# Kernel optimization log

Hardware: AMD Instinct MI355X
Metric: run time of the kernel (lower is better)

## Reference

```python
import jax, jax.numpy as jnp
import numpy as np

B, O, L, E = 8, 4, 1024, 1024
BETA = 512
NSEG = 12
OUT = 1


def setup_inputs() -> dict:
    key = jax.random.key(0)
    ks = jax.random.split(key, 8)
    hidden = jax.random.normal(ks[0], (B, O, L, E), jnp.float32)
    # strictly increasing boundaries in (1, L), shared across the O options (as in the torch code)
    raw = jnp.sort(jax.random.randint(ks[1], (B, NSEG), 2, L - NSEG), axis=-1)
    idx = raw + jnp.arange(NSEG, dtype=raw.dtype)
    s = 0.02
    Wp = jax.random.normal(ks[2], (E, 2 * BETA), jnp.float32) * s
    bp = jnp.zeros((2 * BETA,), jnp.float32)
    Wa0 = jax.random.normal(ks[3], (2 * BETA, BETA), jnp.float32) * s
    ba0 = jnp.zeros((BETA,), jnp.float32)
    Wa = jax.random.normal(ks[4], (BETA, BETA), jnp.float32) * s
    ba = jnp.zeros((BETA,), jnp.float32)
    Wl0 = jax.random.normal(ks[5], (8 * BETA, BETA), jnp.float32) * s
    bl0 = jnp.zeros((BETA,), jnp.float32)
    Wl = jax.random.normal(ks[6], (BETA, OUT), jnp.float32) * s
    bl = jnp.zeros((OUT,), jnp.float32)
    return dict(hidden=hidden, idx=idx, Wp=Wp, bp=bp, Wa0=Wa0, ba0=ba0,
                Wa=Wa, ba=ba, Wl0=Wl0, bl0=bl0, Wl=Wl, bl=bl)


def _seg_mean(P, starts, ends):
    # P: [B,O,L+1,E] exclusive prefix sums; starts/ends: [B,K] token offsets.
    s = jnp.take_along_axis(P, starts[:, None, :, None], axis=2)
    e = jnp.take_along_axis(P, ends[:, None, :, None], axis=2)
    cnt = (ends - starts).astype(P.dtype)[:, None, :, None]
    return (e - s) / cnt  # [B,O,K,E]


def _get_param(x, Wp, bp):
    e = 1.0 + jax.nn.relu(x @ Wp + bp)
    a, b = jnp.split(e, 2, axis=-1)
    return a, b


def _attn_pool(a, b, Wa0, ba0, Wa, ba):
    # attention-weighted reduction over axis -2 (the 'logic' operator)
    h = jax.nn.relu(jnp.concatenate([a, b], axis=-1) @ Wa0 + ba0)
    w = jax.nn.softmax(h @ Wa + ba, axis=-2)
    return (w * a).sum(axis=-2), (w * b).sum(axis=-2)


def reference(hidden, idx, Wp, bp, Wa0, ba0, Wa, ba, Wl0, bl0, Wl, bl):
    # ---- init_embed: ragged segment means via prefix sums (one pass, no host syncs)
    P = jnp.concatenate([jnp.zeros_like(hidden[:, :, :1]),
                         jnp.cumsum(hidden, axis=2)], axis=2)  # [B,O,L+1,E]
    ones = jnp.ones((idx.shape[0], 1), idx.dtype)
    starts_c = jnp.concatenate([ones, idx[:, :NSEG - 3]], axis=1)  # [B, NSEG-2]
    ends_c = idx[:, :NSEG - 2]
    ctx = _seg_mean(P, starts_c, ends_c)                                # [B,O,Nc,E]
    q = _seg_mean(P, idx[:, NSEG - 3:NSEG - 2], idx[:, NSEG - 2:NSEG - 1])[:, :, 0]
    o = _seg_mean(P, idx[:, NSEG - 2:NSEG - 1], idx[:, NSEG - 1:NSEG])[:, :, 0]
    allc = _seg_mean(P, ones, idx[:, NSEG - 3:NSEG - 2])[:, :, 0]       # [B,O,E]
    # ---- beta params for context segments
    a_c, b_c = _get_param(ctx, Wp, bp)                                  # [B,O,Nc,BETA]
    # intersection over segments
    ia, ib = _attn_pool(a_c, b_c, Wa0, ba0, Wa, ba)                     # [B,O,BETA]
    # renew: pair each segment with the intersection, pool over the pair axis
    pa = jnp.stack([a_c, jnp.broadcast_to(ia[:, :, None, :], a_c.shape)], axis=-2)
    pb = jnp.stack([b_c, jnp.broadcast_to(ib[:, :, None, :], b_c.shape)], axis=-2)
    na, nb = _attn_pool(pa, pb, Wa0, ba0, Wa, ba)                       # [B,O,Nc,BETA]
    # union: invert, attention-pool over segments, invert back
    ua, ub = _attn_pool(1.0 / na, 1.0 / nb, Wa0, ba0, Wa, ba)
    ua, ub = 1.0 / ua, 1.0 / ub                                         # [B,O,BETA]
    # ---- beta params for question / option / whole-context spans
    a_q, b_q = _get_param(q, Wp, bp)
    a_o, b_o = _get_param(o, Wp, bp)
    a_ac, b_ac = _get_param(allc, Wp, bp)
    # ---- classify head: concat 4 beta embeddings -> 8*BETA -> MLP -> logits
    cat = jnp.concatenate([ua, ub, a_ac, b_ac, a_o, b_o, a_q, b_q], axis=-1)
    h = jax.nn.relu(cat @ Wl0 + bl0)
    return h @ Wl + bl  # [B,O,OUT]
```

## Files before the change

### kernel.cpp

```cpp
#include <hip/hip_runtime.h>
#include <hip/hip_bf16.h>

#define B_    8
#define O_    4
#define L_    1024
#define E_    1024
#define BETA_ 512
#define NSEG_ 12
#define BO_   32
#define NCH_  16

enum : size_t {
  WS_SPART = 0,
  WS_X     = WS_SPART + (size_t)BO_ * NCH_ * 12 * E_,
  WS_P1P   = WS_X     + (size_t)BO_ * 13 * E_,
  WS_H1P   = WS_P1P   + (size_t)8  * BO_ * 13 * E_,
  WS_T1P   = WS_H1P   + (size_t)16 * BO_ * 10 * BETA_,
  WS_H2P   = WS_T1P   + (size_t)8  * BO_ * 10 * BETA_,
  WS_T2P   = WS_H2P   + (size_t)8  * BO_ * BETA_,
  WS_H3P   = WS_T2P   + (size_t)8  * BO_ * BETA_,
  WS_T3P   = WS_H3P   + (size_t)16 * BO_ * 10 * BETA_,
  WS_HFP   = WS_T3P   + (size_t)8  * BO_ * 10 * BETA_,
  WS_TE    = WS_HFP   + (size_t)32 * BO_ * BETA_,
  WS_T1B   = WS_TE    + (size_t)BO_ * 13 * E_,
  WS_IAB   = WS_T1B   + (size_t)BO_ * 10 * BETA_,
  WS_RN    = WS_IAB   + (size_t)BO_ * 2 * BETA_,
  WS_END   = WS_RN    + (size_t)BO_ * 10 * E_,
};

__device__ __forceinline__ float relu_(float v) { return v > 0.f ? v : 0.f; }

__global__ void k1_segsum(const float* __restrict__ hidden, const int* __restrict__ idx,
                          float* __restrict__ Spart) {
    const int chunk = blockIdx.x;
    const int bo = blockIdx.y;
    const int b = bo >> 2;
    int cuts[13];
    cuts[0] = 1;
#pragma unroll
    for (int i = 0; i < 12; ++i) cuts[i + 1] = idx[b * NSEG_ + i];
    const int e4 = threadIdx.x << 2;
    float* sp = Spart + ((size_t)(bo * NCH_ + chunk) * 12) * E_ + e4;
    const float4 z = make_float4(0.f, 0.f, 0.f, 0.f);
#pragma unroll
    for (int m = 0; m < 12; ++m) *reinterpret_cast<float4*>(sp + (size_t)m * E_) = z;
    const int l0 = chunk * 64;
    const int l1 = l0 + 64;
    int lo = l0 < 1 ? 1 : l0;
    const int hi = l1 < cuts[12] ? l1 : cuts[12];
    if (lo >= hi) return;
    const float* base = hidden + (size_t)bo * (L_ * E_) + e4;
    int j = 0;
    while (j < 11 && cuts[j + 1] <= lo) ++j;
    int l = lo;
    while (l < hi) {
        const int e2 = (j < 11 && cuts[j + 1] < hi) ? cuts[j + 1] : hi;
        float sx = 0.f, sy = 0.f, sz = 0.f, sw = 0.f;
        for (; l < e2; ++l) {
            const float4 v = *reinterpret_cast<const float4*>(base + (size_t)l * E_);
            sx += v.x; sy += v.y; sz += v.z; sw += v.w;
        }
        float4 s; s.x = sx; s.y = sy; s.z = sz; s.w = sw;
        *reinterpret_cast<float4*>(sp + (size_t)j * E_) = s;
        ++j;
    }
}

__global__ __launch_bounds__(256) void k2_means(
    const float* __restrict__ Spart, const int* __restrict__ idx,
    float* __restrict__ X) {
    const int bo = blockIdx.y;
    const int col = blockIdx.x * 256 + threadIdx.x;
    const int b = bo >> 2;
    int cuts[13];
    cuts[0] = 1;
#pragma unroll
    for (int i = 0; i < 12; ++i) cuts[i + 1] = idx[b * NSEG_ + i];
    const float* sp = Spart + (size_t)bo * NCH_ * 12 * E_ + col;
    float allc = 0.f;
#pragma unroll
    for (int m = 0; m < 12; ++m) {
        float s = 0.f;
#pragma unroll
        for (int ch = 0; ch < NCH_; ++ch) s += sp[((size_t)ch * 12 + m) * E_];
        X[((size_t)bo * 13 + m) * E_ + col] = s / (float)(cuts[m + 1] - cuts[m]);
        if (m < 10) allc += s;
    }
    X[((size_t)bo * 13 + 12) * E_ + col] = allc / (float)(cuts[10] - 1);
}

template<int M, int ML, int K, int N, int KC, int BOG, int XF, int NPART>
__global__ __launch_bounds__(256) void gemm_sk(
    const float* __restrict__ Xb, const float* __restrict__ xbias,
    const float* __restrict__ W, float* __restrict__ OUT,
    const float* __restrict__ A0, const float* __restrict__ A1,
    const float* __restrict__ A2, const float* __restrict__ A3,
    float* __restrict__ SIDE, float* __restrict__ SIDE2) {
    const int kidx = blockIdx.x;
    const int k0 = kidx * KC;
    const int bo0 = blockIdx.y * BOG;
    const int c = blockIdx.z * 256 + threadIdx.x;
    const int tid = threadIdx.x;
    __shared__ __align__(16) float xs[BOG * ML * KC];

    for (int i = tid; i < BOG * ML * KC; i += 256) {
        const int kk = i % KC;
        const int rm = i / KC;
        const int m = rm % ML;
        const int bb = rm / ML;
        const int bo = bo0 + bb;
        const int k = k0 + kk;
        float v;
        if constexpr (XF == 0) {
            v = Xb[((size_t)bo * ML + m) * K + k];
        } else if constexpr (XF == 1) {
            float s = xbias[k];
#pragma unroll
            for (int p = 0; p < NPART; ++p)
                s += Xb[(((size_t)p * BO_ + bo) * ML + m) * K + k];
            v = 1.f + relu_(s);
            SIDE[((size_t)bo * ML + m) * K + k] = v;
        } else if constexpr (XF == 2) {
            float s = xbias[k];
#pragma unroll
            for (int p = 0; p < NPART; ++p)
                s += Xb[(((size_t)p * BO_ + bo) * ML + m) * K + k];
            v = relu_(s);
        } else if constexpr (XF == 4) {
            const int col = k & 511, half = k >> 9;
            const float bac = A2[col];
            float t[10], mx = -1e30f;
#pragma unroll
            for (int j = 0; j < 10; ++j) {
                float s = bac;
#pragma unroll
                for (int p = 0; p < NPART; ++p)
                    s += A0[(((size_t)p * BO_ + bo) * 10 + j) * BETA_ + col];
                t[j] = s;
                mx = fmaxf(mx, s);
            }
            if (half == 0) {
#pragma unroll
                for (int j = 0; j < 10; ++j)
                    SIDE2[((size_t)bo * 10 + j) * BETA_ + col] = t[j];
            }
            float sw = 0.f, acc = 0.f;
#pragma unroll
            for (int j = 0; j < 10; ++j) {
                const float pj = expf(t[j] - mx);
                sw += pj;
                acc = fmaf(pj, A1[((size_t)bo * 13 + j) * E_ + half * BETA_ + col], acc);
            }
            v = acc / sw;
            SIDE[(size_t)bo * 1024 + k] = v;
        } else if constexpr (XF == 5) {
            const int col = k & 511, half = k >> 9;
            const float tj = A0[((size_t)bo * 10 + m) * BETA_ + col];
            float tI = A2[col];
#pragma unroll
            for (int p = 0; p < NPART; ++p)
                tI += A1[((size_t)p * BO_ + bo) * BETA_ + col];
            const float mx = fmaxf(tj, tI);
            const float e0 = expf(tj - mx);
            const float e1 = expf(tI - mx);
            const float ea = A3[((size_t)bo * 13 + m) * E_ + half * BETA_ + col];
            const float iv = SIDE2[(size_t)bo * 1024 + k];
            v = (e0 + e1) / (e0 * ea + e1 * iv);
            SIDE[((size_t)bo * 10 + m) * E_ + k] = v;
        } else {
            if (k < 1024) {
                const int col = k & 511, half = k >> 9;
                const float bac = A2[col];
                float t[10], mx = -1e30f;
#pragma unroll
                for (int j = 0; j < 10; ++j) {
                    float s = bac;
#pragma unroll
                    for (int p = 0; p < NPART; ++p)
                        s += A0[(((size_t)p * BO_ + bo) * 10 + j) * BETA_ + col];
                    t[j] = s;
                    mx = fmaxf(mx, s);
                }
                float sw = 0.f, acc = 0.f;
#pragma unroll
                for (int j = 0; j < 10; ++j) {
                    const float pj = expf(t[j] - mx);
                    sw += pj;
                    acc = fmaf(pj, A1[((size_t)bo * 10 + j) * E_ + k], acc);
                }
                v = sw / acc;
            } else {
                const int region = k >> 10;
                const int row = (region == 1) ? 12 : (region == 2) ? 11 : 10;
                v = A3[((size_t)bo * 13 + row) * E_ + (k & 1023)];
            }
        }
        xs[i] = v;
    }
    __syncthreads();

    float acc[BOG][M];
#pragma unroll
    for (int b = 0; b < BOG; ++b)
#pragma unroll
        for (int m = 0; m < M; ++m) acc[b][m] = 0.f;
    const float* __restrict__ wp = W + (size_t)k0 * N + c;
    for (int k4 = 0; k4 < KC / 4; ++k4) {
        const float w0 = wp[(size_t)(4 * k4 + 0) * N];
        const float w1 = wp[(size_t)(4 * k4 + 1) * N];
        const float w2 = wp[(size_t)(4 * k4 + 2) * N];
        const float w3 = wp[(size_t)(4 * k4 + 3) * N];
#pragma unroll
        for (int b = 0; b < BOG; ++b) {
#pragma unroll
            for (int m = 0; m < M; ++m) {
                const float4 xv = *reinterpret_cast<const float4*>(&xs[(b * ML + m) * KC + 4 * k4]);
                float a = acc[b][m];
                a = fmaf(xv.x, w0, a);
                a = fmaf(xv.y, w1, a);
                a = fmaf(xv.z, w2, a);
                a = fmaf(xv.w, w3, a);
                acc[b][m] = a;
            }
        }
    }
#pragma unroll
    for (int b = 0; b < BOG; ++b) {
        float* op = OUT + (((size_t)kidx * BO_ + bo0 + b) * M) * N + c;
#pragma unroll
        for (int m = 0; m < M; ++m) op[(size_t)m * N] = acc[b][m];
    }
}

__global__ void __launch_bounds__(512) k_final(
    const float* __restrict__ HFP, const float* __restrict__ bl0,
    const float* __restrict__ Wl, const float* __restrict__ bl,
    float* __restrict__ out) {
    const int bo = blockIdx.x;
    const int c = threadIdx.x;
    float s = bl0[c];
#pragma unroll
    for (int p = 0; p < 32; ++p) s += HFP[((size_t)p * BO_ + bo) * BETA_ + c];
    float partial = relu_(s) * Wl[c];
#pragma unroll
    for (int off = 32; off > 0; off >>= 1) partial += __shfl_down(partial, off, 64);
    __shared__ float red[8];
    if ((c & 63) == 0) red[c >> 6] = partial;
    __syncthreads();
    if (c == 0) out[bo] = red[0] + red[1] + red[2] + red[3] + red[4] + red[5] + red[6] + red[7] + bl[0];
}

extern "C" void kernel_launch(void* const* d_in, const int* in_sizes, int n_in,
                              void* d_out, int out_size, void* d_ws, size_t ws_size,
                              hipStream_t stream) {
    const float* hidden = (const float*)d_in[0];
    const int* idx = (const int*)d_in[1];
    const float* Wp  = (const float*)d_in[2];
    const float* bp  = (const float*)d_in[3];
    const float* Wa0 = (const float*)d_in[4];
    const float* ba0 = (const float*)d_in[5];
    const float* Wa  = (const float*)d_in[6];
    const float* ba  = (const float*)d_in[7];
    const float* Wl0 = (const float*)d_in[8];
    const float* bl0 = (const float*)d_in[9];
    const float* Wl  = (const float*)d_in[10];
    const float* bl  = (const float*)d_in[11];
    float* ws = (float*)d_ws;
    float* SPART = ws + WS_SPART;
    float* X     = ws + WS_X;
    float* P1P   = ws + WS_P1P;
    float* H1P   = ws + WS_H1P;
    float* T1P   = ws + WS_T1P;
    float* H2P   = ws + WS_H2P;
    float* T2P   = ws + WS_T2P;
    float* H3P   = ws + WS_H3P;
    float* T3P   = ws + WS_T3P;
    float* HFP   = ws + WS_HFP;
    float* TE    = ws + WS_TE;
    float* T1B   = ws + WS_T1B;
    float* IAB   = ws + WS_IAB;
    float* RN    = ws + WS_RN;
    const float* NUL = nullptr;

    k1_segsum<<<dim3(NCH_, BO_), 256, 0, stream>>>(hidden, idx, SPART);
    k2_means<<<dim3(4, BO_), 256, 0, stream>>>(SPART, idx, X);
    gemm_sk<13, 13, 1024, 1024, 128, 2, 0, 1>
        <<<dim3(8, 16, 4), 256, 0, stream>>>(X, NUL, Wp, P1P, NUL, NUL, NUL, NUL, nullptr, nullptr);
    gemm_sk<10, 13, 1024, 512, 64, 2, 1, 8>
        <<<dim3(16, 16, 2), 256, 0, stream>>>(P1P, bp, Wa0, H1P, NUL, NUL, NUL, NUL, TE, nullptr);
    gemm_sk<10, 10, 512, 512, 64, 2, 2, 16>
        <<<dim3(8, 16, 2), 256, 0, stream>>>(H1P, ba0, Wa, T1P, NUL, NUL, NUL, NUL, nullptr, nullptr);
    gemm_sk<1, 1, 1024, 512, 128, 8, 4, 8>
        <<<dim3(8, 4, 2), 256, 0, stream>>>(NUL, NUL, Wa0, H2P, T1P, TE, ba, NUL, IAB, T1B);
    gemm_sk<1, 1, 512, 512, 64, 8, 2, 8>
        <<<dim3(8, 4, 2), 256, 0, stream>>>(H2P, ba0, Wa, T2P, NUL, NUL, NUL, NUL, nullptr, nullptr);
    gemm_sk<10, 10, 1024, 512, 64, 2, 5, 8>
        <<<dim3(16, 16, 2), 256, 0, stream>>>(NUL, NUL, Wa0, H3P, T1B, T2P, ba, TE, RN, IAB);
    gemm_sk<10, 10, 512, 512, 64, 2, 2, 16>
        <<<dim3(8, 16, 2), 256, 0, stream>>>(H3P, ba0, Wa, T3P, NUL, NUL, NUL, NUL, nullptr, nullptr);
    gemm_sk<1, 1, 4096, 512, 128, 8, 6, 8>
        <<<dim3(32, 4, 2), 256, 0, stream>>>(NUL, NUL, Wl0, HFP, T3P, RN, ba, TE, nullptr, nullptr);
    k_final<<<BO_, 512, 0, stream>>>(HFP, bl0, Wl, bl, (float*)d_out);
}
```

Measured before the change: 164.9 us.

## Finer segment-sum chunks and full-N per-block GEMM tiles with more split-K

The segment-sum kernel now uses 64 chunks of 16 rows instead of 16 chunks of 64, dropping the zero-fill of partial buffers and using two independent accumulators per segment. The means kernel sums only the chunks that overlap each segment, so unwritten partials are never read. The GEMMs now have each block cover all N columns, with NC columns per thread and blockIdx.z removed, so the shared-memory X tile is loaded once rather than per column group. They use smaller K chunks and more split-K partitions to keep block counts up. The aim is more parallelism in the bandwidth-bound hidden-state reduction and less redundant X staging, at the cost of more partial-sum traffic and higher register pressure.

After: 550.4 us. 3.34x slower.

```diff
diff --git a/kernel.cpp b/kernel.cpp
--- a/kernel.cpp
+++ b/kernel.cpp
@@ -8,24 +8,24 @@
 #define BETA_ 512
 #define NSEG_ 12
 #define BO_   32
-#define NCH_  16
+#define NCH_  64
 
 enum : size_t {
   WS_SPART = 0,
   WS_X     = WS_SPART + (size_t)BO_ * NCH_ * 12 * E_,
   WS_P1P   = WS_X     + (size_t)BO_ * 13 * E_,
-  WS_H1P   = WS_P1P   + (size_t)8  * BO_ * 13 * E_,
+  WS_TE    = WS_P1P   + (size_t)16 * BO_ * 13 * E_,
+  WS_H1P   = WS_TE    + (size_t)BO_ * 13 * E_,
   WS_T1P   = WS_H1P   + (size_t)16 * BO_ * 10 * BETA_,
-  WS_H2P   = WS_T1P   + (size_t)8  * BO_ * 10 * BETA_,
-  WS_T2P   = WS_H2P   + (size_t)8  * BO_ * BETA_,
-  WS_H3P   = WS_T2P   + (size_t)8  * BO_ * BETA_,
+  WS_T1B   = WS_T1P   + (size_t)16 * BO_ * 10 * BETA_,
+  WS_IAB   = WS_T1B   + (size_t)BO_ * 10 * BETA_,
+  WS_H2P   = WS_IAB   + (size_t)BO_ * 2 * BETA_,
+  WS_T2P   = WS_H2P   + (size_t)16 * BO_ * BETA_,
+  WS_RN    = WS_T2P   + (size_t)16 * BO_ * BETA_,
+  WS_H3P   = WS_RN    + (size_t)BO_ * 10 * E_,
   WS_T3P   = WS_H3P   + (size_t)16 * BO_ * 10 * BETA_,
-  WS_HFP   = WS_T3P   + (size_t)8  * BO_ * 10 * BETA_,
-  WS_TE    = WS_HFP   + (size_t)32 * BO_ * BETA_,
-  WS_T1B   = WS_TE    + (size_t)BO_ * 13 * E_,
-  WS_IAB   = WS_T1B   + (size_t)BO_ * 10 * BETA_,
-  WS_RN    = WS_IAB   + (size_t)BO_ * 2 * BETA_,
-  WS_END   = WS_RN    + (size_t)BO_ * 10 * E_,
+  WS_HFP   = WS_T3P   + (size_t)16 * BO_ * 10 * BETA_,
+  WS_END   = WS_HFP   + (size_t)32 * BO_ * BETA_,
 };
 
 __device__ __forceinline__ float relu_(float v) { return v > 0.f ? v : 0.f; }
@@ -39,28 +39,33 @@
     cuts[0] = 1;
 #pragma unroll
     for (int i = 0; i < 12; ++i) cuts[i + 1] = idx[b * NSEG_ + i];
-    const int e4 = threadIdx.x << 2;
-    float* sp = Spart + ((size_t)(bo * NCH_ + chunk) * 12) * E_ + e4;
-    const float4 z = make_float4(0.f, 0.f, 0.f, 0.f);
-#pragma unroll
-    for (int m = 0; m < 12; ++m) *reinterpret_cast<float4*>(sp + (size_t)m * E_) = z;
-    const int l0 = chunk * 64;
-    const int l1 = l0 + 64;
+    const int l0 = chunk * 16;
+    const int l1 = l0 + 16;
     int lo = l0 < 1 ? 1 : l0;
     const int hi = l1 < cuts[12] ? l1 : cuts[12];
     if (lo >= hi) return;
+    const int e4 = threadIdx.x << 2;
     const float* base = hidden + (size_t)bo * (L_ * E_) + e4;
+    float* sp = Spart + (size_t)(bo * NCH_ + chunk) * 12 * E_ + e4;
     int j = 0;
     while (j < 11 && cuts[j + 1] <= lo) ++j;
     int l = lo;
     while (l < hi) {
         const int e2 = (j < 11 && cuts[j + 1] < hi) ? cuts[j + 1] : hi;
         float sx = 0.f, sy = 0.f, sz = 0.f, sw = 0.f;
-        for (; l < e2; ++l) {
+        float tx = 0.f, ty = 0.f, tz = 0.f, tw = 0.f;
+        for (; l + 1 < e2; l += 2) {
+            const float4 v0 = *reinterpret_cast<const float4*>(base + (size_t)l * E_);
+            const float4 v1 = *reinterpret_cast<const float4*>(base + (size_t)(l + 1) * E_);
+            sx += v0.x; sy += v0.y; sz += v0.z; sw += v0.w;
+            tx += v1.x; ty += v1.y; tz += v1.z; tw += v1.w;
+        }
+        if (l < e2) {
             const float4 v = *reinterpret_cast<const float4*>(base + (size_t)l * E_);
             sx += v.x; sy += v.y; sz += v.z; sw += v.w;
+            ++l;
         }
-        float4 s; s.x = sx; s.y = sy; s.z = sz; s.w = sw;
+        float4 s; s.x = sx + tx; s.y = sy + ty; s.z = sz + tz; s.w = sw + tw;
         *reinterpret_cast<float4*>(sp + (size_t)j * E_) = s;
         ++j;
     }
@@ -80,30 +85,31 @@
     float allc = 0.f;
 #pragma unroll
     for (int m = 0; m < 12; ++m) {
+        const int c0 = cuts[m] >> 4;
+        const int c1 = (cuts[m + 1] - 1) >> 4;
         float s = 0.f;
-#pragma unroll
-        for (int ch = 0; ch < NCH_; ++ch) s += sp[((size_t)ch * 12 + m) * E_];
+        for (int ch = c0; ch <= c1; ++ch) s += sp[((size_t)ch * 12 + m) * E_];
         X[((size_t)bo * 13 + m) * E_ + col] = s / (float)(cuts[m + 1] - cuts[m]);
         if (m < 10) allc += s;
     }
     X[((size_t)bo * 13 + 12) * E_ + col] = allc / (float)(cuts[10] - 1);
 }
 
-template<int M, int ML, int K, int N, int KC, int BOG, int XF, int NPART>
-__global__ __launch_bounds__(256) void gemm_sk(
+template<int M, int ML, int K, int N, int KC, int BOG, int NT, int XF, int NPART>
+__global__ __launch_bounds__(NT) void gemm_nc(
     const float* __restrict__ Xb, const float* __restrict__ xbias,
-    const float* __restrict__ W, float* __restrict__ OUT,
+    const float* __restrict__ W, float* __restrict__ OUTP,
     const float* __restrict__ A0, const float* __restrict__ A1,
     const float* __restrict__ A2, const float* __restrict__ A3,
     float* __restrict__ SIDE, float* __restrict__ SIDE2) {
+    constexpr int NC = N / NT;
     const int kidx = blockIdx.x;
     const int k0 = kidx * KC;
     const int bo0 = blockIdx.y * BOG;
-    const int c = blockIdx.z * 256 + threadIdx.x;
     const int tid = threadIdx.x;
     __shared__ __align__(16) float xs[BOG * ML * KC];
 
-    for (int i = tid; i < BOG * ML * KC; i += 256) {
+    for (int i = tid; i < BOG * ML * KC; i += NT) {
         const int kk = i % KC;
         const int rm = i / KC;
         const int m = rm % ML;
@@ -169,7 +175,7 @@
             SIDE[((size_t)bo * 10 + m) * E_ + k] = v;
         } else {
             if (k < 1024) {
-                const int col = k & 511, half = k >> 9;
+                const int col = k & 511;
                 const float bac = A2[col];
                 float t[10], mx = -1e30f;
 #pragma unroll
@@ -199,36 +205,45 @@
     }
     __syncthreads();
 
-    float acc[BOG][M];
+    float acc[BOG][M][NC];
 #pragma unroll
     for (int b = 0; b < BOG; ++b)
 #pragma unroll
-        for (int m = 0; m < M; ++m) acc[b][m] = 0.f;
-    const float* __restrict__ wp = W + (size_t)k0 * N + c;
+        for (int m = 0; m < M; ++m)
+#pragma unroll
+            for (int q = 0; q < NC; ++q) acc[b][m][q] = 0.f;
+    const float* __restrict__ wp = W + (size_t)k0 * N + tid;
     for (int k4 = 0; k4 < KC / 4; ++k4) {
-        const float w0 = wp[(size_t)(4 * k4 + 0) * N];
-        const float w1 = wp[(size_t)(4 * k4 + 1) * N];
-        const float w2 = wp[(size_t)(4 * k4 + 2) * N];
-        const float w3 = wp[(size_t)(4 * k4 + 3) * N];
+        float w[4][NC];
+#pragma unroll
+        for (int kk = 0; kk < 4; ++kk)
+#pragma unroll
+            for (int q = 0; q < NC; ++q)
+                w[kk][q] = wp[(size_t)(4 * k4 + kk) * N + q * NT];
 #pragma unroll
         for (int b = 0; b < BOG; ++b) {
 #pragma unroll
             for (int m = 0; m < M; ++m) {
                 const float4 xv = *reinterpret_cast<const float4*>(&xs[(b * ML + m) * KC + 4 * k4]);
-                float a = acc[b][m];
-                a = fmaf(xv.x, w0, a);
-                a = fmaf(xv.y, w1, a);
-                a = fmaf(xv.z, w2, a);
-                a = fmaf(xv.w, w3, a);
-                acc[b][m] = a;
+#pragma unroll
+                for (int q = 0; q < NC; ++q) {
+                    float a = acc[b][m][q];
+                    a = fmaf(xv.x, w[0][q], a);
+                    a = fmaf(xv.y, w[1][q], a);
+                    a = fmaf(xv.z, w[2][q], a);
+                    a = fmaf(xv.w, w[3][q], a);
+                    acc[b][m][q] = a;
+                }
             }
         }
     }
 #pragma unroll
     for (int b = 0; b < BOG; ++b) {
-        float* op = OUT + (((size_t)kidx * BO_ + bo0 + b) * M) * N + c;
-#pragma unroll
-        for (int m = 0; m < M; ++m) op[(size_t)m * N] = acc[b][m];
+        float* op = OUTP + (((size_t)kidx * BO_ + bo0 + b) * M) * N + tid;
+#pragma unroll
+        for (int m = 0; m < M; ++m)
+#pragma unroll
+            for (int q = 0; q < NC; ++q) op[(size_t)m * N + q * NT] = acc[b][m][q];
     }
 }
 
@@ -269,36 +284,36 @@
     float* SPART = ws + WS_SPART;
     float* X     = ws + WS_X;
     float* P1P   = ws + WS_P1P;
+    float* TE    = ws + WS_TE;
     float* H1P   = ws + WS_H1P;
     float* T1P   = ws + WS_T1P;
+    float* T1B   = ws + WS_T1B;
+    float* IAB   = ws + WS_IAB;
     float* H2P   = ws + WS_H2P;
     float* T2P   = ws + WS_T2P;
+    float* RN    = ws + WS_RN;
     float* H3P   = ws + WS_H3P;
     float* T3P   = ws + WS_T3P;
     float* HFP   = ws + WS_HFP;
-    float* TE    = ws + WS_TE;
-    float* T1B   = ws + WS_T1B;
-    float* IAB   = ws + WS_IAB;
-    float* RN    = ws + WS_RN;
     const float* NUL = nullptr;
 
     k1_segsum<<<dim3(NCH_, BO_), 256, 0, stream>>>(hidden, idx, SPART);
     k2_means<<<dim3(4, BO_), 256, 0, stream>>>(SPART, idx, X);
-    gemm_sk<13, 13, 1024, 1024, 128, 2, 0, 1>
-        <<<dim3(8, 16, 4), 256, 0, stream>>>(X, NUL, Wp, P1P, NUL, NUL, NUL, NUL, nullptr, nullptr);
-    gemm_sk<10, 13, 1024, 512, 64, 2, 1, 8>
-        <<<dim3(16, 16, 2), 256, 0, stream>>>(P1P, bp, Wa0, H1P, NUL, NUL, NUL, NUL, TE, nullptr);
-    gemm_sk<10, 10, 512, 512, 64, 2, 2, 16>
-        <<<dim3(8, 16, 2), 256, 0, stream>>>(H1P, ba0, Wa, T1P, NUL, NUL, NUL, NUL, nullptr, nullptr);
-    gemm_sk<1, 1, 1024, 512, 128, 8, 4, 8>
-        <<<dim3(8, 4, 2), 256, 0, stream>>>(NUL, NUL, Wa0, H2P, T1P, TE, ba, NUL, IAB, T1B);
-    gemm_sk<1, 1, 512, 512, 64, 8, 2, 8>
-        <<<dim3(8, 4, 2), 256, 0, stream>>>(H2P, ba0, Wa, T2P, NUL, NUL, NUL, NUL, nullptr, nullptr);
-    gemm_sk<10, 10, 1024, 512, 64, 2, 5, 8>
-        <<<dim3(16, 16, 2), 256, 0, stream>>>(NUL, NUL, Wa0, H3P, T1B, T2P, ba, TE, RN, IAB);
-    gemm_sk<10, 10, 512, 512, 64, 2, 2, 16>
-        <<<dim3(8, 16, 2), 256, 0, stream>>>(H3P, ba0, Wa, T3P, NUL, NUL, NUL, NUL, nullptr, nullptr);
-    gemm_sk<1, 1, 4096, 512, 128, 8, 6, 8>
-        <<<dim3(32, 4, 2), 256, 0, stream>>>(NUL, NUL, Wl0, HFP, T3P, RN, ba, TE, nullptr, nullptr);
+    gemm_nc<13, 13, 1024, 1024, 64, 2, 256, 0, 1>
+        <<<dim3(16, 16), 256, 0, stream>>>(X, NUL, Wp, P1P, NUL, NUL, NUL, NUL, nullptr, nullptr);
+    gemm_nc<10, 13, 1024, 512, 64, 2, 128, 1, 16>
+        <<<dim3(16, 16), 128, 0, stream>>>(P1P, bp, Wa0, H1P, NUL, NUL, NUL, NUL, TE, nullptr);
+    gemm_nc<10, 10, 512, 512, 32, 2, 128, 2, 16>
+        <<<dim3(16, 16), 128, 0, stream>>>(H1P, ba0, Wa, T1P, NUL, NUL, NUL, NUL, nullptr, nullptr);
+    gemm_nc<1, 1, 1024, 512, 64, 8, 128, 4, 16>
+        <<<dim3(16, 4), 128, 0, stream>>>(NUL, NUL, Wa0, H2P, T1P, TE, ba, NUL, IAB, T1B);
+    gemm_nc<1, 1, 512, 512, 32, 8, 128, 2, 16>
+        <<<dim3(16, 4), 128, 0, stream>>>(H2P, ba0, Wa, T2P, NUL, NUL, NUL, NUL, nullptr, nullptr);
+    gemm_nc<10, 10, 1024, 512, 64, 2, 128, 5, 16>
+        <<<dim3(16, 16), 128, 0, stream>>>(NUL, NUL, Wa0, H3P, T1B, T2P, ba, TE, RN, IAB);
+    gemm_nc<10, 10, 512, 512, 32, 2, 128, 2, 16>
+        <<<dim3(16, 16), 128, 0, stream>>>(H3P, ba0, Wa, T3P, NUL, NUL, NUL, NUL, nullptr, nullptr);
+    gemm_nc<1, 1, 4096, 512, 128, 8, 128, 6, 16>
+        <<<dim3(32, 4), 128, 0, stream>>>(NUL, NUL, Wl0, HFP, T3P, RN, ba, TE, nullptr, nullptr);
     k_final<<<BO_, 512, 0, stream>>>(HFP, bl0, Wl, bl, (float*)d_out);
 }
```

## Split softmax-pool prologues out of GEMM staging into separate small kernels

Applied to the files above, without the earlier changes.

The attention softmax pooling that was recomputed inside the X-staging prologue of two split-K GEMMs (every column tile redid the 10-way softmax for its k chunk) moves into dedicated kernels, t_iab and t_cat. These write their pooled vectors to workspace once, and the GEMMs then load plain X. This removes redundant exp/reduction work repeated across N-tiles, at the cost of two extra launches and a round trip through global memory. The first projection GEMM also changes its BO grouping from 2 to 4 and halves its grid.

New measurement: 178.8 us. 8.4% more time.

```diff
diff --git a/kernel.cpp b/kernel.cpp
--- a/kernel.cpp
+++ b/kernel.cpp
@@ -25,7 +25,8 @@
   WS_T1B   = WS_TE    + (size_t)BO_ * 13 * E_,
   WS_IAB   = WS_T1B   + (size_t)BO_ * 10 * BETA_,
   WS_RN    = WS_IAB   + (size_t)BO_ * 2 * BETA_,
-  WS_END   = WS_RN    + (size_t)BO_ * 10 * E_,
+  WS_CAT   = WS_RN    + (size_t)BO_ * 10 * E_,
+  WS_END   = WS_CAT   + (size_t)BO_ * 8 * BETA_,
 };
 
 __device__ __forceinline__ float relu_(float v) { return v > 0.f ? v : 0.f; }
@@ -126,34 +127,7 @@
             for (int p = 0; p < NPART; ++p)
                 s += Xb[(((size_t)p * BO_ + bo) * ML + m) * K + k];
             v = relu_(s);
-        } else if constexpr (XF == 4) {
-            const int col = k & 511, half = k >> 9;
-            const float bac = A2[col];
-            float t[10], mx = -1e30f;
-#pragma unroll
-            for (int j = 0; j < 10; ++j) {
-                float s = bac;
-#pragma unroll
-                for (int p = 0; p < NPART; ++p)
-                    s += A0[(((size_t)p * BO_ + bo) * 10 + j) * BETA_ + col];
-                t[j] = s;
-                mx = fmaxf(mx, s);
-            }
-            if (half == 0) {
-#pragma unroll
-                for (int j = 0; j < 10; ++j)
-                    SIDE2[((size_t)bo * 10 + j) * BETA_ + col] = t[j];
-            }
-            float sw = 0.f, acc = 0.f;
-#pragma unroll
-            for (int j = 0; j < 10; ++j) {
-                const float pj = expf(t[j] - mx);
-                sw += pj;
-                acc = fmaf(pj, A1[((size_t)bo * 13 + j) * E_ + half * BETA_ + col], acc);
-            }
-            v = acc / sw;
-            SIDE[(size_t)bo * 1024 + k] = v;
-        } else if constexpr (XF == 5) {
+        } else {
             const int col = k & 511, half = k >> 9;
             const float tj = A0[((size_t)bo * 10 + m) * BETA_ + col];
             float tI = A2[col];
@@ -167,33 +141,6 @@
             const float iv = SIDE2[(size_t)bo * 1024 + k];
             v = (e0 + e1) / (e0 * ea + e1 * iv);
             SIDE[((size_t)bo * 10 + m) * E_ + k] = v;
-        } else {
-            if (k < 1024) {
-                const int col = k & 511, half = k >> 9;
-                const float bac = A2[col];
-                float t[10], mx = -1e30f;
-#pragma unroll
-                for (int j = 0; j < 10; ++j) {
-                    float s = bac;
-#pragma unroll
-                    for (int p = 0; p < NPART; ++p)
-                        s += A0[(((size_t)p * BO_ + bo) * 10 + j) * BETA_ + col];
-                    t[j] = s;
-                    mx = fmaxf(mx, s);
-                }
-                float sw = 0.f, acc = 0.f;
-#pragma unroll
-                for (int j = 0; j < 10; ++j) {
-                    const float pj = expf(t[j] - mx);
-                    sw += pj;
-                    acc = fmaf(pj, A1[((size_t)bo * 10 + j) * E_ + k], acc);
-                }
-                v = sw / acc;
-            } else {
-                const int region = k >> 10;
-                const int row = (region == 1) ? 12 : (region == 2) ? 11 : 10;
-                v = A3[((size_t)bo * 13 + row) * E_ + (k & 1023)];
-            }
         }
         xs[i] = v;
     }
@@ -230,6 +177,73 @@
 #pragma unroll
         for (int m = 0; m < M; ++m) op[(size_t)m * N] = acc[b][m];
     }
+}
+
+__global__ void __launch_bounds__(512) t_iab(
+    const float* __restrict__ T1P, const float* __restrict__ ba,
+    const float* __restrict__ TE, float* __restrict__ T1B,
+    float* __restrict__ IAB) {
+    const int bo = blockIdx.x;
+    const int c = threadIdx.x;
+    const float bac = ba[c];
+    float t[10], mx = -1e30f;
+#pragma unroll
+    for (int j = 0; j < 10; ++j) {
+        float s = bac;
+#pragma unroll
+        for (int p = 0; p < 8; ++p)
+            s += T1P[(((size_t)p * BO_ + bo) * 10 + j) * BETA_ + c];
+        t[j] = s;
+        T1B[((size_t)bo * 10 + j) * BETA_ + c] = s;
+        mx = fmaxf(mx, s);
+    }
+    float p[10], sw = 0.f;
+#pragma unroll
+    for (int j = 0; j < 10; ++j) { p[j] = expf(t[j] - mx); sw += p[j]; }
+    float ia = 0.f, ib = 0.f;
+#pragma unroll
+    for (int j = 0; j < 10; ++j) {
+        ia = fmaf(p[j], TE[((size_t)bo * 13 + j) * E_ + c], ia);
+        ib = fmaf(p[j], TE[((size_t)bo * 13 + j) * E_ + BETA_ + c], ib);
+    }
+    IAB[(size_t)bo * 1024 + c] = ia / sw;
+    IAB[(size_t)bo * 1024 + BETA_ + c] = ib / sw;
+}
+
+__global__ __launch_bounds__(256) void t_cat(
+    const float* __restrict__ T3P, const float* __restrict__ ba,
+    const float* __restrict__ RN, const float* __restrict__ TE,
+    float* __restrict__ CAT) {
+    const int bo = blockIdx.y;
+    const int k = blockIdx.x * 256 + threadIdx.x;
+    float v;
+    if (k < 1024) {
+        const int col = k & 511;
+        const float bac = ba[col];
+        float t[10], mx = -1e30f;
+#pragma unroll
+        for (int j = 0; j < 10; ++j) {
+            float s = bac;
+#pragma unroll
+            for (int p = 0; p < 8; ++p)
+                s += T3P[(((size_t)p * BO_ + bo) * 10 + j) * BETA_ + col];
+            t[j] = s;
+            mx = fmaxf(mx, s);
+        }
+        float sw = 0.f, acc = 0.f;
+#pragma unroll
+        for (int j = 0; j < 10; ++j) {
+            const float pj = expf(t[j] - mx);
+            sw += pj;
+            acc = fmaf(pj, RN[((size_t)bo * 10 + j) * E_ + k], acc);
+        }
+        v = sw / acc;
+    } else {
+        const int region = k >> 10;
+        const int row = (region == 1) ? 12 : (region == 2) ? 11 : 10;
+        v = TE[((size_t)bo * 13 + row) * E_ + (k & 1023)];
+    }
+    CAT[(size_t)bo * 4096 + k] = v;
 }
 
 __global__ void __launch_bounds__(512) k_final(
@@ -280,25 +294,28 @@
     float* T1B   = ws + WS_T1B;
     float* IAB   = ws + WS_IAB;
     float* RN    = ws + WS_RN;
+    float* CAT   = ws + WS_CAT;
     const float* NUL = nullptr;
 
     k1_segsum<<<dim3(NCH_, BO_), 256, 0, stream>>>(hidden, idx, SPART);
     k2_means<<<dim3(4, BO_), 256, 0, stream>>>(SPART, idx, X);
-    gemm_sk<13, 13, 1024, 1024, 128, 2, 0, 1>
-        <<<dim3(8, 16, 4), 256, 0, stream>>>(X, NUL, Wp, P1P, NUL, NUL, NUL, NUL, nullptr, nullptr);
+    gemm_sk<13, 13, 1024, 1024, 128, 4, 0, 1>
+        <<<dim3(8, 8, 4), 256, 0, stream>>>(X, NUL, Wp, P1P, NUL, NUL, NUL, NUL, nullptr, nullptr);
     gemm_sk<10, 13, 1024, 512, 64, 2, 1, 8>
         <<<dim3(16, 16, 2), 256, 0, stream>>>(P1P, bp, Wa0, H1P, NUL, NUL, NUL, NUL, TE, nullptr);
     gemm_sk<10, 10, 512, 512, 64, 2, 2, 16>
         <<<dim3(8, 16, 2), 256, 0, stream>>>(H1P, ba0, Wa, T1P, NUL, NUL, NUL, NUL, nullptr, nullptr);
-    gemm_sk<1, 1, 1024, 512, 128, 8, 4, 8>
-        <<<dim3(8, 4, 2), 256, 0, stream>>>(NUL, NUL, Wa0, H2P, T1P, TE, ba, NUL, IAB, T1B);
+    t_iab<<<BO_, 512, 0, stream>>>(T1P, ba, TE, T1B, IAB);
+    gemm_sk<1, 1, 1024, 512, 128, 8, 0, 1>
+        <<<dim3(8, 4, 2), 256, 0, stream>>>(IAB, NUL, Wa0, H2P, NUL, NUL, NUL, NUL, nullptr, nullptr);
     gemm_sk<1, 1, 512, 512, 64, 8, 2, 8>
         <<<dim3(8, 4, 2), 256, 0, stream>>>(H2P, ba0, Wa, T2P, NUL, NUL, NUL, NUL, nullptr, nullptr);
     gemm_sk<10, 10, 1024, 512, 64, 2, 5, 8>
         <<<dim3(16, 16, 2), 256, 0, stream>>>(NUL, NUL, Wa0, H3P, T1B, T2P, ba, TE, RN, IAB);
     gemm_sk<10, 10, 512, 512, 64, 2, 2, 16>
         <<<dim3(8, 16, 2), 256, 0, stream>>>(H3P, ba0, Wa, T3P, NUL, NUL, NUL, NUL, nullptr, nullptr);
-    gemm_sk<1, 1, 4096, 512, 128, 8, 6, 8>
-        <<<dim3(32, 4, 2), 256, 0, stream>>>(NUL, NUL, Wl0, HFP, T3P, RN, ba, TE, nullptr, nullptr);
+    t_cat<<<dim3(16, BO_), 256, 0, stream>>>(T3P, ba, RN, TE, CAT);
+    gemm_sk<1, 1, 4096, 512, 128, 8, 0, 1>
+        <<<dim3(32, 4, 2), 256, 0, stream>>>(CAT, NUL, Wl0, HFP, NUL, NUL, NUL, NUL, nullptr, nullptr);
     k_final<<<BO_, 512, 0, stream>>>(HFP, bl0, Wl, bl, (float*)d_out);
 }
```
